# Optimization experiments

Measured on AMD Instinct MI355X. Metric: run time of the kernel, lower is better.

The kernel has to match this reference:

```python
import jax, jax.numpy as jnp
import numpy as np

VOCAB = 256   # == tagset_size (char-level CRF)
EMB = 512
HID = 1024
H = HID // 2  # per-direction hidden
T = 4096
START = 0
STOP = 1
NEG = -10000.0


def setup_inputs() -> dict:
    key = jax.random.key(0)
    ks = jax.random.split(key, 14)
    s = 0.05
    trans = jax.random.normal(ks[12], (VOCAB, VOCAB), dtype=jnp.float32)
    trans = trans.at[START, :].set(NEG).at[:, STOP].set(NEG)
    return {
        "src": jax.random.randint(ks[0], (T, 1), 0, VOCAB),
        "lengths": T,
        "embedding": jax.random.normal(ks[1], (VOCAB, EMB), dtype=jnp.float32) * s,
        "W_ih_f": jax.random.normal(ks[2], (4 * H, EMB), dtype=jnp.float32) * s,
        "W_hh_f": jax.random.normal(ks[3], (4 * H, H), dtype=jnp.float32) * s,
        "b_ih_f": jax.random.normal(ks[4], (4 * H,), dtype=jnp.float32) * s,
        "b_hh_f": jax.random.normal(ks[5], (4 * H,), dtype=jnp.float32) * s,
        "W_ih_b": jax.random.normal(ks[6], (4 * H, EMB), dtype=jnp.float32) * s,
        "W_hh_b": jax.random.normal(ks[7], (4 * H, H), dtype=jnp.float32) * s,
        "b_ih_b": jax.random.normal(ks[8], (4 * H,), dtype=jnp.float32) * s,
        "b_hh_b": jax.random.normal(ks[9], (4 * H,), dtype=jnp.float32) * s,
        "W_tag": jax.random.normal(ks[10], (VOCAB, HID), dtype=jnp.float32) * s,
        "b_tag": jax.random.normal(ks[11], (VOCAB,), dtype=jnp.float32) * s,
        "transitions": trans,
    }


def _lstm_dir(x, W_ih, W_hh, b_ih, b_hh, reverse):
    # x: [T, B, E] -> hs: [T, B, H]. PyTorch gate order: i, f, g, o.
    Hd = W_hh.shape[1]
    h0 = jnp.zeros((x.shape[1], Hd), x.dtype)

    def step(carry, x_t):
        h, c = carry
        g = x_t @ W_ih.T + b_ih + h @ W_hh.T + b_hh
        i, f, gg, o = jnp.split(g, 4, axis=-1)
        c = jax.nn.sigmoid(f) * c + jax.nn.sigmoid(i) * jnp.tanh(gg)
        h = jax.nn.sigmoid(o) * jnp.tanh(c)
        return (h, c), h

    _, hs = jax.lax.scan(step, (h0, h0), x, reverse=reverse)
    return hs


def reference(src, lengths, embedding, W_ih_f, W_hh_f, b_ih_f, b_hh_f,
              W_ih_b, W_hh_b, b_ih_b, b_hh_b, W_tag, b_tag, transitions):
    # Embedding (dropout is identity in eval mode); batch = 1 as in the torch code.
    x = embedding[src]  # [T, 1, EMB]
    hf = _lstm_dir(x, W_ih_f, W_hh_f, b_ih_f, b_hh_f, False)
    hb = _lstm_dir(x, W_ih_b, W_hh_b, b_ih_b, b_hh_b, True)
    out = jnp.concatenate([hf, hb], axis=-1)          # [T, 1, HID]
    feats = out @ W_tag.T + b_tag                     # [T, 1, K]
    f = feats[:, 0, :]                                # [T, K]
    K = transitions.shape[0]

    fv0 = jnp.full((K,), NEG, f.dtype).at[START].set(0.0)

    def vstep(fv, feat):
        scores = fv[None, :] + transitions            # [next, prev]
        bp = jnp.argmax(scores, axis=1)
        return jnp.max(scores, axis=1) + feat, bp

    fv, bps = jax.lax.scan(vstep, fv0, f)             # bps: [T, K]
    term = fv + transitions[STOP]
    best = jnp.argmax(term)
    score = term[best]

    def bt(tag, bp):
        return bp[tag], tag

    _, path = jax.lax.scan(bt, best, bps, reverse=True)  # [T], path[t] = best tag at t
    return score, path
```

## Files before the change

### kernel.cpp

```cpp
#include <hip/hip_runtime.h>
#include <stdint.h>

#define T_LEN 4096
#define NVOC 256
#define EMBD 512
#define HID 512
#define G4 2048
#define NEGV (-10000.0f)
#define START_TAG 0
#define STOP_TAG 1

typedef float f4 __attribute__((ext_vector_type(4)));
typedef unsigned int u32x4 __attribute__((ext_vector_type(4)));

#define BAR_LGKM() do { \
    asm volatile("s_waitcnt lgkmcnt(0)\n\ts_barrier" ::: "memory"); \
    __builtin_amdgcn_sched_barrier(0); \
} while (0)

__global__ __launch_bounds__(256) void gemm_abt(
    const float* __restrict__ A, const float* __restrict__ B,
    const float* __restrict__ bias0, const float* __restrict__ bias1,
    float* __restrict__ C, int M, int N, int K)
{
    __shared__ float As[16][65];
    __shared__ float Bs[16][65];
    int m0 = blockIdx.x * 64, n0 = blockIdx.y * 64;
    int tid = threadIdx.x;
    int lr = tid >> 2;
    int lk = (tid & 3) << 2;
    int tr = tid & 15, tc = tid >> 4;
    float acc[4][4] = {};
    for (int k0 = 0; k0 < K; k0 += 16) {
        float4 av = *(const float4*)(A + (size_t)(m0 + lr) * K + k0 + lk);
        float4 bv = *(const float4*)(B + (size_t)(n0 + lr) * K + k0 + lk);
        As[lk + 0][lr] = av.x; As[lk + 1][lr] = av.y; As[lk + 2][lr] = av.z; As[lk + 3][lr] = av.w;
        Bs[lk + 0][lr] = bv.x; Bs[lk + 1][lr] = bv.y; Bs[lk + 2][lr] = bv.z; Bs[lk + 3][lr] = bv.w;
        __syncthreads();
#pragma unroll
        for (int kk = 0; kk < 16; ++kk) {
            float a[4], b[4];
#pragma unroll
            for (int x = 0; x < 4; ++x) a[x] = As[kk][tr * 4 + x];
#pragma unroll
            for (int y = 0; y < 4; ++y) b[y] = Bs[kk][tc * 4 + y];
#pragma unroll
            for (int y = 0; y < 4; ++y)
#pragma unroll
                for (int x = 0; x < 4; ++x)
                    acc[y][x] += a[x] * b[y];
        }
        __syncthreads();
    }
#pragma unroll
    for (int y = 0; y < 4; ++y) {
        int n = n0 + tc * 4 + y;
        float bb = bias0 ? bias0[n] : 0.f;
        if (bias1) bb += bias1[n];
#pragma unroll
        for (int x = 0; x < 4; ++x)
            C[(size_t)(m0 + tr * 4 + x) * N + n] = acc[y][x] + bb;
    }
}

__device__ __forceinline__ float fast_sig(float x) {
    return __builtin_amdgcn_rcpf(1.f + __expf(-x));
}
__device__ __forceinline__ float fast_tanh(float x) {
    return 2.f * __builtin_amdgcn_rcpf(1.f + __expf(-2.f * x)) - 1.f;
}

__global__ __launch_bounds__(512, 1) void lstm_kernel(
    const int* __restrict__ src,
    const float* __restrict__ PE_f, const float* __restrict__ PE_b,
    const float* __restrict__ Whh_f, const float* __restrict__ Whh_b,
    float* __restrict__ H, unsigned long long* __restrict__ pub)
{
    int wg  = blockIdx.x & 31;
    int dir = blockIdx.x >> 5;
    const float* PE  = dir ? PE_b : PE_f;
    const float* Whh = dir ? Whh_b : Whh_f;
    unsigned long long* mypub = pub + (size_t)dir * 1024;

    int tid = threadIdx.x;
    int q = tid & 7;
    int g = (tid >> 3) & 3;
    int u = tid >> 5;
    int hu0 = wg * 16;
    int grow = g * 512 + hu0 + u;

    const f4* wsrc = (const f4*)(Whh + (size_t)grow * 512 + q * 64);
    f4 w00 = wsrc[0],  w01 = wsrc[1],  w02 = wsrc[2],  w03 = wsrc[3];
    f4 w04 = wsrc[4],  w05 = wsrc[5],  w06 = wsrc[6],  w07 = wsrc[7];
    f4 w08 = wsrc[8],  w09 = wsrc[9],  w10 = wsrc[10], w11 = wsrc[11];
    f4 w12 = wsrc[12], w13 = wsrc[13], w14 = wsrc[14], w15 = wsrc[15];
    asm volatile("" : "+v"(w00), "+v"(w01), "+v"(w02), "+v"(w03),
                      "+v"(w04), "+v"(w05), "+v"(w06), "+v"(w07),
                      "+v"(w08), "+v"(w09), "+v"(w10), "+v"(w11),
                      "+v"(w12), "+v"(w13), "+v"(w14), "+v"(w15));

    __shared__ __align__(16) float h_sh[2][8][68];
    float c_state = 0.f;
    bool leader = ((tid & 31) == 0);
    bool q0 = (q == 0);
    bool poller = (tid < 64);

    int st_nxt = src[dir ? (T_LEN - 2) : 1];
    float pe_cur = 0.f;
    if (q0) {
        int st0 = src[dir ? (T_LEN - 1) : 0];
        pe_cur = PE[(size_t)st0 * G4 + grow];
    }

    for (int s = 0; s < T_LEN; ++s) {
        int par = s & 1;
        int t = dir ? (T_LEN - 1 - s) : s;

        float pe_nxt = 0.f;
        if (q0) pe_nxt = PE[(size_t)st_nxt * G4 + grow];
        int s2 = (s + 2 < T_LEN) ? (s + 2) : (T_LEN - 1);
        int st_n2 = src[dir ? (T_LEN - 1 - s2) : s2];

        if (s == 0) {
            h_sh[0][tid >> 6][tid & 63] = 0.f;
        } else if (poller) {
            const char* base = (const char*)(mypub + (size_t)((s - 1) & 1) * 512);
            const char* adr0 = base + tid * 16;
            unsigned int want = (unsigned)s;
            u32x4 a0, a1, a2, a3;
            for (;;) {
                asm volatile(
                    "global_load_dwordx4 %0, %4, off sc0 sc1\n\t"
                    "global_load_dwordx4 %1, %5, off sc0 sc1\n\t"
                    "global_load_dwordx4 %2, %6, off sc0 sc1\n\t"
                    "global_load_dwordx4 %3, %7, off sc0 sc1\n\t"
                    "s_waitcnt vmcnt(0)"
                    : "=&v"(a0), "=&v"(a1), "=&v"(a2), "=&v"(a3)
                    : "v"(adr0), "v"(adr0 + 1024), "v"(adr0 + 2048), "v"(adr0 + 3072)
                    : "memory");
                bool ok = (a0.y >= want) & (a0.w >= want)
                        & (a1.y >= want) & (a1.w >= want)
                        & (a2.y >= want) & (a2.w >= want)
                        & (a3.y >= want) & (a3.w >= want);
                if (ok) break;
                __builtin_amdgcn_s_sleep(1);
            }
            int col = (2 * tid) & 63, rb = tid >> 5;
            float2* d0 = (float2*)&h_sh[par][0 + rb][col];
            float2* d1 = (float2*)&h_sh[par][2 + rb][col];
            float2* d2 = (float2*)&h_sh[par][4 + rb][col];
            float2* d3 = (float2*)&h_sh[par][6 + rb][col];
            *d0 = make_float2(__uint_as_float(a0.x), __uint_as_float(a0.z));
            *d1 = make_float2(__uint_as_float(a1.x), __uint_as_float(a1.z));
            *d2 = make_float2(__uint_as_float(a2.x), __uint_as_float(a2.z));
            *d3 = make_float2(__uint_as_float(a3.x), __uint_as_float(a3.z));
        }
        BAR_LGKM();

        const f4* hq = (const f4*)(&h_sh[par][q][0]);
        f4 acc = {0.f, 0.f, 0.f, 0.f};
#define ACC(W,J) { f4 hv = hq[J]; acc += W * hv; }
        ACC(w00,0)  ACC(w01,1)  ACC(w02,2)  ACC(w03,3)
        ACC(w04,4)  ACC(w05,5)  ACC(w06,6)  ACC(w07,7)
        ACC(w08,8)  ACC(w09,9)  ACC(w10,10) ACC(w11,11)
        ACC(w12,12) ACC(w13,13) ACC(w14,14) ACC(w15,15)
#undef ACC
        float dot = (acc.x + acc.y) + (acc.z + acc.w);
        dot += __shfl_xor(dot, 1);
        dot += __shfl_xor(dot, 2);
        dot += __shfl_xor(dot, 4);
        float val = dot + pe_cur;
        int base_l = tid & ~31;
        float vf = __shfl(val, base_l + 8);
        float vg = __shfl(val, base_l + 16);
        float vo = __shfl(val, base_l + 24);
        if (leader) {
            float si = fast_sig(val);
            float sf = fast_sig(vf);
            float tg = fast_tanh(vg);
            float so = fast_sig(vo);
            c_state = sf * c_state + si * tg;
            float hval = so * fast_tanh(c_state);
            unsigned int hb; __builtin_memcpy(&hb, &hval, 4);
            unsigned long long wv = ((unsigned long long)(unsigned)(s + 1) << 32) | (unsigned long long)hb;
            __hip_atomic_store(mypub + (size_t)par * 512 + hu0 + u, wv,
                               __ATOMIC_RELAXED, __HIP_MEMORY_SCOPE_AGENT);
            H[(size_t)t * 1024 + dir * 512 + hu0 + u] = hval;
        }
        pe_cur = pe_nxt;
        st_nxt = st_n2;
    }
}

__global__ __launch_bounds__(512, 1) void viterbi_fwd_kernel(
    const float* __restrict__ feats, const float* __restrict__ trans,
    float* __restrict__ fv_all)
{
    __shared__ __align__(16) float fvb[2][256];
    int tid = threadIdx.x;
    int wv = tid >> 6;
    int l  = tid & 63;
    int h  = l >> 5;
    int jj = l & 31;
    int j  = wv * 32 + jj;
    const f4* tr = (const f4*)(trans + (size_t)j * 256 + h * 128);
    f4 T00 = tr[0],  T01 = tr[1],  T02 = tr[2],  T03 = tr[3];
    f4 T04 = tr[4],  T05 = tr[5],  T06 = tr[6],  T07 = tr[7];
    f4 T08 = tr[8],  T09 = tr[9],  T10 = tr[10], T11 = tr[11];
    f4 T12 = tr[12], T13 = tr[13], T14 = tr[14], T15 = tr[15];
    f4 T16 = tr[16], T17 = tr[17], T18 = tr[18], T19 = tr[19];
    f4 T20 = tr[20], T21 = tr[21], T22 = tr[22], T23 = tr[23];
    f4 T24 = tr[24], T25 = tr[25], T26 = tr[26], T27 = tr[27];
    f4 T28 = tr[28], T29 = tr[29], T30 = tr[30], T31 = tr[31];
    asm volatile("" : "+v"(T00), "+v"(T01), "+v"(T02), "+v"(T03),
                      "+v"(T04), "+v"(T05), "+v"(T06), "+v"(T07),
                      "+v"(T08), "+v"(T09), "+v"(T10), "+v"(T11),
                      "+v"(T12), "+v"(T13), "+v"(T14), "+v"(T15));
    asm volatile("" : "+v"(T16), "+v"(T17), "+v"(T18), "+v"(T19),
                      "+v"(T20), "+v"(T21), "+v"(T22), "+v"(T23),
                      "+v"(T24), "+v"(T25), "+v"(T26), "+v"(T27),
                      "+v"(T28), "+v"(T29), "+v"(T30), "+v"(T31));
    if (tid < 256) fvb[0][tid] = (tid == START_TAG) ? 0.f : NEGV;
    bool h0 = (h == 0);
    float ft_next = h0 ? feats[j] : 0.f;
    __syncthreads();
    for (int t = 0; t < T_LEN; ++t) {
        int p = t & 1;
        float ft = ft_next;
        if (h0 && t + 1 < T_LEN) ft_next = feats[(size_t)(t + 1) * 256 + j];
        const f4* fq = (const f4*)(&fvb[p][h * 128]);
        f4 mv0 = {-1e30f, -1e30f, -1e30f, -1e30f};
        f4 mv1 = mv0, mv2 = mv0, mv3 = mv0;
#define VSTEP(W,K,MV) { f4 sv = fq[K] + W; MV = __builtin_elementwise_max(MV, sv); }
        VSTEP(T00,0,mv0)  VSTEP(T01,1,mv1)  VSTEP(T02,2,mv2)  VSTEP(T03,3,mv3)
        VSTEP(T04,4,mv0)  VSTEP(T05,5,mv1)  VSTEP(T06,6,mv2)  VSTEP(T07,7,mv3)
        VSTEP(T08,8,mv0)  VSTEP(T09,9,mv1)  VSTEP(T10,10,mv2) VSTEP(T11,11,mv3)
        VSTEP(T12,12,mv0) VSTEP(T13,13,mv1) VSTEP(T14,14,mv2) VSTEP(T15,15,mv3)
        VSTEP(T16,16,mv0) VSTEP(T17,17,mv1) VSTEP(T18,18,mv2) VSTEP(T19,19,mv3)
        VSTEP(T20,20,mv0) VSTEP(T21,21,mv1) VSTEP(T22,22,mv2) VSTEP(T23,23,mv3)
        VSTEP(T24,24,mv0) VSTEP(T25,25,mv1) VSTEP(T26,26,mv2) VSTEP(T27,27,mv3)
        VSTEP(T28,28,mv0) VSTEP(T29,29,mv1) VSTEP(T30,30,mv2) VSTEP(T31,31,mv3)
#undef VSTEP
        f4 mv = __builtin_elementwise_max(__builtin_elementwise_max(mv0, mv1),
                                          __builtin_elementwise_max(mv2, mv3));
        float m = fmaxf(fmaxf(mv.x, mv.y), fmaxf(mv.z, mv.w));
        m = fmaxf(m, __shfl_xor(m, 32));
        if (h0) {
            float v = m + ft;
            fvb[p ^ 1][j] = v;
            fv_all[(size_t)t * 256 + j] = v;
        }
        BAR_LGKM();
    }
}

__global__ __launch_bounds__(256) void transpose_kernel(
    const float* __restrict__ in, float* __restrict__ out)
{
    __shared__ float tile[16][17];
    int bx = blockIdx.x & 15, by = blockIdx.x >> 4;
    int tx = threadIdx.x & 15, ty = threadIdx.x >> 4;
    tile[ty][tx] = in[(size_t)(by * 16 + ty) * 256 + bx * 16 + tx];
    __syncthreads();
    out[(size_t)(bx * 16 + ty) * 256 + by * 16 + tx] = tile[tx][ty];
}

__global__ __launch_bounds__(256) void bp_kernel(
    const float* __restrict__ fv_all, const float* __restrict__ transT,
    unsigned char* __restrict__ bp)
{
    __shared__ float fp[256];
    int t = blockIdx.x;
    int j = threadIdx.x;
    fp[j] = (t == 0) ? ((j == START_TAG) ? 0.f : NEGV)
                     : fv_all[(size_t)(t - 1) * 256 + j];
    __syncthreads();
    float m = -1e30f; int mi = 0;
#pragma unroll 4
    for (int i = 0; i < 256; ++i) {
        float s = fp[i] + transT[(size_t)i * 256 + j];
        if (s > m) { m = s; mi = i; }
    }
    bp[(size_t)t * 256 + j] = (unsigned char)mi;
}

__global__ __launch_bounds__(256) void evol_kernel(
    const unsigned char* __restrict__ bp, unsigned char* __restrict__ evol)
{
    __shared__ unsigned char tm[256];
    __shared__ unsigned char row[256];
    int s = blockIdx.x;
    int tid = threadIdx.x;
    int t_top = s * 64 + 63;
    tm[tid] = (unsigned char)tid;
    evol[(size_t)t_top * 256 + tid] = (unsigned char)tid;
    __syncthreads();
    for (int t = t_top - 1; t >= s * 64; --t) {
        row[tid] = bp[(size_t)(t + 1) * 256 + tid];
        __syncthreads();
        unsigned char nt = row[tm[tid]];
        tm[tid] = nt;
        evol[(size_t)t * 256 + tid] = nt;
        __syncthreads();
    }
}

__global__ __launch_bounds__(256) void finalize_kernel(
    const float* __restrict__ fv_all, const float* __restrict__ trans,
    const unsigned char* __restrict__ bp, const unsigned char* __restrict__ evol,
    float* __restrict__ out)
{
    __shared__ float term[256];
    __shared__ unsigned char top[64];
    int tid = threadIdx.x;
    term[tid] = fv_all[(size_t)(T_LEN - 1) * 256 + tid] + trans[STOP_TAG * 256 + tid];
    __syncthreads();
    if (tid == 0) {
        float m = term[0]; int best = 0;
        for (int i = 1; i < 256; ++i) if (term[i] > m) { m = term[i]; best = i; }
        out[0] = m;
        int tag = best;
        top[63] = (unsigned char)tag;
        for (int s2 = 63; s2 >= 1; --s2) {
            int tb = s2 * 64;
            int pb = evol[(size_t)tb * 256 + tag];
            tag = bp[(size_t)tb * 256 + pb];
            top[s2 - 1] = (unsigned char)tag;
        }
    }
    __syncthreads();
    for (int t = tid; t < T_LEN; t += 256)
        out[1 + t] = (float)evol[(size_t)t * 256 + top[t >> 6]];
}

extern "C" void kernel_launch(void* const* d_in, const int* in_sizes, int n_in,
                              void* d_out, int out_size, void* d_ws, size_t ws_size,
                              hipStream_t stream)
{
    const int*   src     = (const int*)d_in[0];
    const float* emb     = (const float*)d_in[2];
    const float* W_ih_f  = (const float*)d_in[3];
    const float* W_hh_f  = (const float*)d_in[4];
    const float* b_ih_f  = (const float*)d_in[5];
    const float* b_hh_f  = (const float*)d_in[6];
    const float* W_ih_b  = (const float*)d_in[7];
    const float* W_hh_b  = (const float*)d_in[8];
    const float* b_ih_b  = (const float*)d_in[9];
    const float* b_hh_b  = (const float*)d_in[10];
    const float* W_tag   = (const float*)d_in[11];
    const float* b_tag   = (const float*)d_in[12];
    const float* trans   = (const float*)d_in[13];
    float* out = (float*)d_out;

    char* w = (char*)d_ws;
    unsigned long long* pub = (unsigned long long*)w;
    size_t off = 32768;
    float* PE_f = (float*)(w + off); off += (size_t)NVOC * G4 * 4;
    float* PE_b = (float*)(w + off); off += (size_t)NVOC * G4 * 4;
    float* H    = (float*)(w + off); off += (size_t)T_LEN * 1024 * 4;
    float* feats= (float*)(w + off); off += (size_t)T_LEN * 256 * 4;
    float* fv   = (float*)(w + off); off += (size_t)T_LEN * 256 * 4;
    float* transT = (float*)(w + off); off += (size_t)256 * 256 * 4;
    unsigned char* bp   = (unsigned char*)(w + off); off += (size_t)T_LEN * 256;
    unsigned char* evol = (unsigned char*)(w + off); off += (size_t)T_LEN * 256;

    hipMemsetAsync(pub, 0, 16384, stream);

    gemm_abt<<<dim3(NVOC / 64, G4 / 64), 256, 0, stream>>>(emb, W_ih_f, b_ih_f, b_hh_f, PE_f, NVOC, G4, EMBD);
    gemm_abt<<<dim3(NVOC / 64, G4 / 64), 256, 0, stream>>>(emb, W_ih_b, b_ih_b, b_hh_b, PE_b, NVOC, G4, EMBD);
    transpose_kernel<<<256, 256, 0, stream>>>(trans, transT);

    lstm_kernel<<<64, 512, 0, stream>>>(src, PE_f, PE_b, W_hh_f, W_hh_b, H, pub);

    gemm_abt<<<dim3(T_LEN / 64, 256 / 64), 256, 0, stream>>>(H, W_tag, b_tag, nullptr, feats, T_LEN, 256, 1024);

    viterbi_fwd_kernel<<<1, 512, 0, stream>>>(feats, trans, fv);
    bp_kernel<<<T_LEN, 256, 0, stream>>>(fv, transT, bp);
    evol_kernel<<<T_LEN / 64, 256, 0, stream>>>(bp, evol);
    finalize_kernel<<<1, 256, 0, stream>>>(fv, trans, bp, evol, out);
}
```

Measured before the change: 10.88 ms.

## Replace per-step workgroup barrier with LDS flag and double-buffered polling

Removes the s_barrier each LSTM step. Wave 0 instead polls the published hidden state for the next step and writes it into shared memory, then sets an LDS step flag that the other waves spin on. Polling keeps two batches of loads in flight without sleeping, so the next slice is picked up sooner. The costs are busy-spinning waves and a memory-ordering risk: waves can run ahead reading h_sh while wave 0 is still writing the other buffer.

```diff
diff --git a/kernel.cpp b/kernel.cpp
--- a/kernel.cpp
+++ b/kernel.cpp
@@ -70,6 +70,23 @@
     return 2.f * __builtin_amdgcn_rcpf(1.f + __expf(-2.f * x)) - 1.f;
 }
 
+#define ISSUE_POLL(R0, R1, R2, R3) \
+    asm volatile("global_load_dwordx4 %0, %4, off sc0 sc1\n\t" \
+                 "global_load_dwordx4 %1, %5, off sc0 sc1\n\t" \
+                 "global_load_dwordx4 %2, %6, off sc0 sc1\n\t" \
+                 "global_load_dwordx4 %3, %7, off sc0 sc1" \
+                 : "=&v"(R0), "=&v"(R1), "=&v"(R2), "=&v"(R3) \
+                 : "v"(a0), "v"(a1), "v"(a2), "v"(a3) : "memory")
+
+#define WAIT_BLOCK() do { \
+    asm volatile("s_waitcnt vmcnt(4)" ::: "memory"); \
+    __builtin_amdgcn_sched_barrier(0); \
+} while (0)
+
+#define TAGS_OK(R0, R1, R2, R3) \
+    ((R0.y >= want) & (R0.w >= want) & (R1.y >= want) & (R1.w >= want) & \
+     (R2.y >= want) & (R2.w >= want) & (R3.y >= want) & (R3.w >= want))
+
 __global__ __launch_bounds__(512, 1) void lstm_kernel(
     const int* __restrict__ src,
     const float* __restrict__ PE_f, const float* __restrict__ PE_b,
@@ -94,68 +111,35 @@
     f4 w04 = wsrc[4],  w05 = wsrc[5],  w06 = wsrc[6],  w07 = wsrc[7];
     f4 w08 = wsrc[8],  w09 = wsrc[9],  w10 = wsrc[10], w11 = wsrc[11];
     f4 w12 = wsrc[12], w13 = wsrc[13], w14 = wsrc[14], w15 = wsrc[15];
-    asm volatile("" : "+v"(w00), "+v"(w01), "+v"(w02), "+v"(w03),
-                      "+v"(w04), "+v"(w05), "+v"(w06), "+v"(w07),
-                      "+v"(w08), "+v"(w09), "+v"(w10), "+v"(w11),
-                      "+v"(w12), "+v"(w13), "+v"(w14), "+v"(w15));
 
     __shared__ __align__(16) float h_sh[2][8][68];
+    __shared__ int step_flag;
     float c_state = 0.f;
     bool leader = ((tid & 31) == 0);
     bool q0 = (q == 0);
-    bool poller = (tid < 64);
+    bool w0 = (tid < 64);
+
+    h_sh[0][tid >> 6][tid & 63] = 0.f;
+    if (tid == 0) step_flag = 0;
+    __syncthreads();
 
     int st_nxt = src[dir ? (T_LEN - 2) : 1];
     float pe_cur = 0.f;
-    if (q0) {
-        int st0 = src[dir ? (T_LEN - 1) : 0];
-        pe_cur = PE[(size_t)st0 * G4 + grow];
-    }
+    if (q0) pe_cur = PE[(size_t)src[dir ? (T_LEN - 1) : 0] * G4 + grow];
+
+    volatile int* fl = &step_flag;
 
     for (int s = 0; s < T_LEN; ++s) {
         int par = s & 1;
         int t = dir ? (T_LEN - 1 - s) : s;
+
+        while (*fl < s) {}
+        __builtin_amdgcn_sched_barrier(0);
 
         float pe_nxt = 0.f;
         if (q0) pe_nxt = PE[(size_t)st_nxt * G4 + grow];
         int s2 = (s + 2 < T_LEN) ? (s + 2) : (T_LEN - 1);
         int st_n2 = src[dir ? (T_LEN - 1 - s2) : s2];
-
-        if (s == 0) {
-            h_sh[0][tid >> 6][tid & 63] = 0.f;
-        } else if (poller) {
-            const char* base = (const char*)(mypub + (size_t)((s - 1) & 1) * 512);
-            const char* adr0 = base + tid * 16;
-            unsigned int want = (unsigned)s;
-            u32x4 a0, a1, a2, a3;
-            for (;;) {
-                asm volatile(
-                    "global_load_dwordx4 %0, %4, off sc0 sc1\n\t"
-                    "global_load_dwordx4 %1, %5, off sc0 sc1\n\t"
-                    "global_load_dwordx4 %2, %6, off sc0 sc1\n\t"
-                    "global_load_dwordx4 %3, %7, off sc0 sc1\n\t"
-                    "s_waitcnt vmcnt(0)"
-                    : "=&v"(a0), "=&v"(a1), "=&v"(a2), "=&v"(a3)
-                    : "v"(adr0), "v"(adr0 + 1024), "v"(adr0 + 2048), "v"(adr0 + 3072)
-                    : "memory");
-                bool ok = (a0.y >= want) & (a0.w >= want)
-                        & (a1.y >= want) & (a1.w >= want)
-                        & (a2.y >= want) & (a2.w >= want)
-                        & (a3.y >= want) & (a3.w >= want);
-                if (ok) break;
-                __builtin_amdgcn_s_sleep(1);
-            }
-            int col = (2 * tid) & 63, rb = tid >> 5;
-            float2* d0 = (float2*)&h_sh[par][0 + rb][col];
-            float2* d1 = (float2*)&h_sh[par][2 + rb][col];
-            float2* d2 = (float2*)&h_sh[par][4 + rb][col];
-            float2* d3 = (float2*)&h_sh[par][6 + rb][col];
-            *d0 = make_float2(__uint_as_float(a0.x), __uint_as_float(a0.z));
-            *d1 = make_float2(__uint_as_float(a1.x), __uint_as_float(a1.z));
-            *d2 = make_float2(__uint_as_float(a2.x), __uint_as_float(a2.z));
-            *d3 = make_float2(__uint_as_float(a3.x), __uint_as_float(a3.z));
-        }
-        BAR_LGKM();
 
         const f4* hq = (const f4*)(&h_sh[par][q][0]);
         f4 acc = {0.f, 0.f, 0.f, 0.f};
@@ -189,6 +173,40 @@
         }
         pe_cur = pe_nxt;
         st_nxt = st_n2;
+
+        if (w0 && s + 1 < T_LEN) {
+            unsigned int want = (unsigned)(s + 1);
+            const char* sb = par ? (const char*)(mypub + 512) : (const char*)mypub;
+            const char* a0 = sb + tid * 16;
+            const char* a1 = a0 + 1024;
+            const char* a2 = a0 + 2048;
+            const char* a3 = a0 + 3072;
+            u32x4 A0, A1, A2, A3, B0, B1, B2, B3;
+            ISSUE_POLL(A0, A1, A2, A3);
+            ISSUE_POLL(B0, B1, B2, B3);
+            bool useB = false;
+            for (;;) {
+                WAIT_BLOCK();
+                if (__all(TAGS_OK(A0, A1, A2, A3))) break;
+                ISSUE_POLL(A0, A1, A2, A3);
+                WAIT_BLOCK();
+                if (__all(TAGS_OK(B0, B1, B2, B3))) { useB = true; break; }
+                ISSUE_POLL(B0, B1, B2, B3);
+            }
+            u32x4 r0 = useB ? B0 : A0;
+            u32x4 r1 = useB ? B1 : A1;
+            u32x4 r2 = useB ? B2 : A2;
+            u32x4 r3 = useB ? B3 : A3;
+            int col = (2 * tid) & 63, rb = tid >> 5;
+            int np = (s + 1) & 1;
+            *(float2*)&h_sh[np][0 + rb][col] = make_float2(__uint_as_float(r0.x), __uint_as_float(r0.z));
+            *(float2*)&h_sh[np][2 + rb][col] = make_float2(__uint_as_float(r1.x), __uint_as_float(r1.z));
+            *(float2*)&h_sh[np][4 + rb][col] = make_float2(__uint_as_float(r2.x), __uint_as_float(r2.z));
+            *(float2*)&h_sh[np][6 + rb][col] = make_float2(__uint_as_float(r3.x), __uint_as_float(r3.z));
+            asm volatile("s_waitcnt lgkmcnt(0)" ::: "memory");
+            __builtin_amdgcn_sched_barrier(0);
+            if (tid == 0) *fl = s + 1;
+        }
     }
 }
 
```

After: 15.80 ms. 1.45x slower.
